# Kernel optimization log

Hardware: AMD Instinct MI355X
Metric: run time of the kernel (lower is better)

The kernel has to match this reference:

```python
import jax, jax.numpy as jnp
import numpy as np

C_CURV = 1.0          # Poincare ball curvature
EPS = 1e-5
MAX_NORM = (1.0 - 1e-4) / np.sqrt(C_CURV)


def _artanh(x):
    x = jnp.clip(x, -1.0 + 1e-5, 1.0 - 1e-5)
    return 0.5 * (jnp.log1p(x) - jnp.log1p(-x))


def _expmap0(v):
    # v: [N,C,H,W]; norm over channel dim per spatial location
    n = jnp.maximum(jnp.linalg.norm(v, axis=1, keepdims=True), EPS)
    sc = np.sqrt(C_CURV)
    return jnp.tanh(sc * n) * v / (sc * n)


def _logmap0(y):
    n = jnp.maximum(jnp.linalg.norm(y, axis=1, keepdims=True), EPS)
    sc = np.sqrt(C_CURV)
    return _artanh(sc * n) * y / (sc * n)


def _project(y):
    # clamp back inside the ball
    n = jnp.maximum(jnp.linalg.norm(y, axis=1, keepdims=True), EPS)
    return jnp.where(n > MAX_NORM, y * (MAX_NORM / n), y)


def _conv3x3(u, w, b):
    y = jax.lax.conv_general_dilated(u, w, window_strides=(1, 1),
                                     padding=((1, 1), (1, 1)),
                                     dimension_numbers=('NCHW', 'OIHW', 'NCHW'))
    return y + b[None, :, None, None]


def _hconv(x, w, b):
    # HConvolution2d: tangent-space conv around origin
    return _project(_expmap0(_conv3x3(_logmap0(x), w, b)))


def _hbn(x, gamma, beta):
    # HBatchNorm2d: Euclidean BN in the tangent space at the origin (training stats)
    u = _logmap0(x)
    m = u.mean(axis=(0, 2, 3), keepdims=True)
    v = u.var(axis=(0, 2, 3), keepdims=True)
    u = (u - m) / jnp.sqrt(v + 1e-5)
    u = u * gamma[None, :, None, None] + beta[None, :, None, None]
    return _project(_expmap0(u))


def _hrelu(x):
    return _project(_expmap0(jax.nn.relu(_logmap0(x))))


def setup_inputs() -> dict:
    key = jax.random.key(0)
    ks = jax.random.split(key, 8)
    N, Cin, Cmid, Cout, H, W = 8, 32, 32, 32, 256, 256
    # input point on the Poincare ball
    x = _project(_expmap0(0.1 * jax.random.normal(ks[0], (N, Cin, H, W), jnp.float32)))
    fan1 = Cin * 9
    fan2 = Cmid * 9
    w1 = jax.random.normal(ks[1], (Cmid, Cin, 3, 3), jnp.float32) / np.sqrt(fan1)
    b1 = jnp.zeros((Cmid,), jnp.float32)
    g1 = jnp.ones((Cmid,), jnp.float32)
    beta1 = jnp.zeros((Cmid,), jnp.float32)
    w2 = jax.random.normal(ks[2], (Cout, Cmid, 3, 3), jnp.float32) / np.sqrt(fan2)
    b2 = jnp.zeros((Cout,), jnp.float32)
    g2 = jnp.ones((Cout,), jnp.float32)
    beta2 = jnp.zeros((Cout,), jnp.float32)
    return {"x": x, "w1": w1, "b1": b1, "g1": g1, "beta1": beta1,
            "w2": w2, "b2": b2, "g2": g2, "beta2": beta2}


def reference(x, w1, b1, g1, beta1, w2, b2, g2, beta2):
    out = _hconv(x, w1, b1)
    out = _hbn(out, g1, beta1)
    out = _hrelu(out)
    out = _hconv(out, w2, b2)
    out = _hbn(out, g2, beta2)
    out = _hrelu(out)
    return out
```

## Files before the change

### kernel.cpp

```cpp
#include <hip/hip_runtime.h>
#include <math.h>

#define HWDIM 256
#define CH 32
#define NB 8
#define TILE 16
#define NLOC (NB*HWDIM*HWDIM)
#define R_CLAMP 4.9517189f
#define MAXN 0.9999f
#define BN_EPS 1e-5f
#define EPSF 1e-5f
#define TPB 2
#define GRIDC 1024
#define OST 264

typedef __attribute__((ext_vector_type(8))) _Float16 half8;
typedef __attribute__((ext_vector_type(4))) _Float16 half4;
typedef __attribute__((ext_vector_type(4))) float floatx4;

__device__ __forceinline__ float artanh_fast(float n) {
    float t = fminf(n, 1.0f - 1e-5f);
    return 0.5f * __logf(__fdividef(1.0f + t, 1.0f - t));
}

__global__ __launch_bounds__(256) void wprep_kernel(
    const float* __restrict__ w1, const float* __restrict__ w2,
    _Float16* __restrict__ wp1, _Float16* __restrict__ wp2)
{
    int idx = blockIdx.x * 256 + threadIdx.x;
    if (idx >= 2*CH*CH*9) return;
    int s = idx >= CH*CH*9;
    int id = idx - s*(CH*CH*9);
    const float* w = s ? w2 : w1;
    _Float16* wp = s ? wp2 : wp1;
    int j  = id & 7;
    int r  = id >> 3;
    int co = r & 31;
    int og = r >> 5;
    int g  = og & 3;
    int o  = og >> 2;
    int ci = g*8 + j;
    wp[id] = (_Float16)w[(co*CH + ci)*9 + o];
}

template<int STAGE>
__device__ __forceinline__ void stage_loc(const void* __restrict__ srcv, int bz,
                                          int gh, int gw, bool inb,
                                          _Float16* base, const float* __restrict__ scsh)
{
    if (!inb) {
        half8 z = {0,0,0,0,0,0,0,0};
        #pragma unroll
        for (int g = 0; g < 4; g++) *(half8*)(base + g*144) = z;
        return;
    }
    float v[CH]; float n2 = 0.f;
    if (STAGE == 1) {
        const float* p = (const float*)srcv + ((size_t)bz*CH << 16) + gh*HWDIM + gw;
        #pragma unroll
        for (int c = 0; c < CH; c++) { float t0 = p[(size_t)c << 16]; v[c] = t0; n2 = fmaf(t0, t0, n2); }
        float n = fmaxf(sqrtf(n2), EPSF);
        float f = __fdividef(artanh_fast(n), n);
        #pragma unroll
        for (int g = 0; g < 4; g++) {
            half8 hv;
            #pragma unroll
            for (int j = 0; j < 8; j++) hv[j] = (_Float16)(v[g*8 + j] * f);
            *(half8*)(base + g*144) = hv;
        }
    } else {
        const _Float16* p = (const _Float16*)srcv + (((size_t)bz << 16) + gh*HWDIM + gw)*CH;
        half8 raw[4];
        #pragma unroll
        for (int k = 0; k < 4; k++) raw[k] = *(const half8*)(p + 8*k);
        #pragma unroll
        for (int c = 0; c < CH; c++) {
            float t0 = fmaf((float)raw[c>>3][c&7], scsh[c], scsh[CH + c]);
            v[c] = t0; n2 = fmaf(t0, t0, n2);
        }
        float n = sqrtf(n2);
        float f = (n > R_CLAMP) ? __fdividef(R_CLAMP, n) : 1.0f;
        #pragma unroll
        for (int g = 0; g < 4; g++) {
            half8 hv;
            #pragma unroll
            for (int j = 0; j < 8; j++) hv[j] = (_Float16)fmaxf(v[g*8 + j]*f, 0.0f);
            *(half8*)(base + g*144) = hv;
        }
    }
}

template<int STAGE>
__global__ __launch_bounds__(256) void conv_mfma_kernel(
    const void* __restrict__ srcv,
    const _Float16* __restrict__ wp,
    const float* __restrict__ bias,
    const float* __restrict__ scsh,
    _Float16* __restrict__ dst,
    float* __restrict__ partials)
{
    __shared__ _Float16 ah[10368];
    __shared__ float red[4][64];

    const int tid = threadIdx.x;
    const int b   = blockIdx.x;
    const int bz  = b & 7;
    const int tb  = b >> 3;
    const int by  = tb >> 3;
    const int bx0 = (tb & 7) * TPB;
    const int h0  = by*TILE - 1;
    const int wbase = bx0*TILE - 1;

    const int sy0 = tid / 18, sx0 = tid - sy0*18;
    const int gh0 = h0 + sy0;
    const bool row0 = (gh0 >= 0) & (gh0 < HWDIM);
    const bool has1 = tid < 68;
    const int l1 = tid + 256;
    const int sy1 = l1 / 18, sx1 = l1 - sy1*18;
    const int gh1 = h0 + sy1;
    const bool row1 = has1 & (gh1 >= 0) & (gh1 < HWDIM);
    _Float16* const base0 = ah + ((sy0*4)*18 + sx0)*8;
    _Float16* const base1 = ah + ((sy1*4)*18 + sx1)*8;

    const int lane = tid & 63, wave = tid >> 6;
    const int xx = lane & 15, q = lane >> 4;

    float bs[8];
    #pragma unroll
    for (int r = 0; r < 4; r++) { bs[r] = bias[q*4+r]; bs[4+r] = bias[q*4+r+16]; }
    float sv[8], qv[8];
    #pragma unroll
    for (int k = 0; k < 8; k++) { sv[k] = 0.f; qv[k] = 0.f; }

    #pragma unroll 1
    for (int j = 0; j < TPB; j++) {
        {
            int gw0 = wbase + j*TILE + sx0;
            bool in0 = row0 & (gw0 >= 0) & (gw0 < HWDIM);
            stage_loc<STAGE>(srcv, bz, gh0, gw0, in0, base0, scsh);
        }
        if (has1) {
            int gw1 = wbase + j*TILE + sx1;
            bool in1 = row1 & (gw1 >= 0) & (gw1 < HWDIM);
            stage_loc<STAGE>(srcv, bz, gh1, gw1, in1, base1, scsh);
        }
        __syncthreads();

        floatx4 acc[4][2];
        #pragma unroll
        for (int i = 0; i < 4; i++) {
            acc[i][0] = (floatx4){0.f,0.f,0.f,0.f};
            acc[i][1] = (floatx4){0.f,0.f,0.f,0.f};
        }
        __builtin_amdgcn_s_setprio(1);
        #pragma unroll
        for (int dx = 0; dx < 3; dx++) {
            half8 af[6];
            #pragma unroll
            for (int yy = 0; yy < 6; yy++)
                af[yy] = *(const half8*)(ah + (((wave*4+yy)*4 + q)*18 + xx + dx)*8);
            #pragma unroll
            for (int dy = 0; dy < 3; dy++) {
                const int o = dy*3 + dx;
                const _Float16* wb = wp + (size_t)((o*4 + q)*32)*8;
                half8 wf0 = *(const half8*)(wb + xx*8);
                half8 wf1 = *(const half8*)(wb + (xx+16)*8);
                #pragma unroll
                for (int i = 0; i < 4; i++) {
                    acc[i][0] = __builtin_amdgcn_mfma_f32_16x16x32_f16(wf0, af[i+dy], acc[i][0], 0,0,0);
                    acc[i][1] = __builtin_amdgcn_mfma_f32_16x16x32_f16(wf1, af[i+dy], acc[i][1], 0,0,0);
                }
            }
        }
        __builtin_amdgcn_s_setprio(0);

        _Float16* dp = dst + (((size_t)bz << 16) + (size_t)(by*TILE)*HWDIM + (bx0 + j)*TILE + xx)*CH + q*4;
        #pragma unroll
        for (int i = 0; i < 4; i++) {
            float n2 = 0.f;
            #pragma unroll
            for (int r = 0; r < 4; r++) {
                acc[i][0][r] += bs[r];
                acc[i][1][r] += bs[4+r];
                n2 = fmaf(acc[i][0][r], acc[i][0][r], n2);
                n2 = fmaf(acc[i][1][r], acc[i][1][r], n2);
            }
            n2 += __shfl_xor(n2, 16, 64);
            n2 += __shfl_xor(n2, 32, 64);
            float nn = sqrtf(n2);
            float f = (nn > R_CLAMP) ? __fdividef(R_CLAMP, nn) : 1.0f;
            half4 o0, o1;
            #pragma unroll
            for (int r = 0; r < 4; r++) {
                float a0 = acc[i][0][r] * f;
                float a1 = acc[i][1][r] * f;
                sv[r]   += a0; qv[r]   = fmaf(a0, a0, qv[r]);
                sv[4+r] += a1; qv[4+r] = fmaf(a1, a1, qv[4+r]);
                o0[r] = (_Float16)a0; o1[r] = (_Float16)a1;
            }
            _Float16* a = dp + (size_t)(wave*4 + i)*HWDIM*CH;
            *(half4*)(a)      = o0;
            *(half4*)(a + 16) = o1;
        }
        __syncthreads();
    }

    #pragma unroll
    for (int k = 0; k < 8; k++) {
        #pragma unroll
        for (int m = 1; m < 16; m <<= 1) {
            sv[k] += __shfl_xor(sv[k], m, 64);
            qv[k] += __shfl_xor(qv[k], m, 64);
        }
    }
    if (xx == 0) {
        #pragma unroll
        for (int r = 0; r < 4; r++) {
            red[wave][q*4+r]        = sv[r];
            red[wave][16 + q*4+r]   = sv[4+r];
            red[wave][32 + q*4+r]   = qv[r];
            red[wave][48 + q*4+r]   = qv[4+r];
        }
    }
    __syncthreads();
    if (tid < 64) {
        float s = red[0][tid] + red[1][tid] + red[2][tid] + red[3][tid];
        partials[(size_t)tid*GRIDC + b] = s;
    }
}

__global__ __launch_bounds__(256) void finalize_kernel(
    const float* __restrict__ partials,
    const float* __restrict__ g, const float* __restrict__ beta,
    float* __restrict__ scsh)
{
    __shared__ float ss[256], sq[256];
    const int c = blockIdx.x;
    const int tid = threadIdx.x;
    float s = 0.f, q = 0.f;
    for (int b = tid; b < GRIDC; b += 256) {
        s += partials[(size_t)c*GRIDC + b];
        q += partials[(size_t)(CH + c)*GRIDC + b];
    }
    ss[tid] = s; sq[tid] = q;
    __syncthreads();
    for (int st = 128; st > 0; st >>= 1) {
        if (tid < st) { ss[tid] += ss[tid+st]; sq[tid] += sq[tid+st]; }
        __syncthreads();
    }
    if (tid == 0) {
        const float NS = (float)NLOC;
        float mean = ss[0] / NS;
        float var = fmaxf(sq[0] / NS - mean*mean, 0.0f);
        float sc = g[c] / sqrtf(var + BN_EPS);
        scsh[c] = sc;
        scsh[CH + c] = beta[c] - mean*sc;
    }
}

__global__ __launch_bounds__(256) void out_kernel(
    const _Float16* __restrict__ t4c, const float* __restrict__ scsh,
    float* __restrict__ out)
{
    __shared__ float outb[16*OST];
    const int w = threadIdx.x;
    const int h = blockIdx.x, n = blockIdx.y;
    const _Float16* p = t4c + (((size_t)n << 16) + (size_t)h*HWDIM + w)*CH;
    half8 raw[4];
    #pragma unroll
    for (int k = 0; k < 4; k++) raw[k] = *(const half8*)(p + 8*k);
    float u[CH]; float n2 = 0.f;
    #pragma unroll
    for (int c = 0; c < CH; c++) {
        float t = fmaf((float)raw[c>>3][c&7], scsh[c], scsh[CH+c]);
        u[c] = t; n2 = fmaf(t, t, n2);
    }
    float nn = sqrtf(n2);
    float f = (nn > R_CLAMP) ? __fdividef(R_CLAMP, nn) : 1.0f;
    float r2 = 0.f;
    #pragma unroll
    for (int c = 0; c < CH; c++) { float r = fmaxf(u[c]*f, 0.0f); u[c] = r; r2 = fmaf(r, r, r2); }
    float rn = fmaxf(sqrtf(r2), EPSF);
    float a = __expf(2.0f * rn);
    float th = __fdividef(a - 1.0f, a + 1.0f);
    float s = __fdividef(fminf(th, MAXN), rn);
    #pragma unroll
    for (int c = 0; c < CH; c++) u[c] *= s;

    #pragma unroll
    for (int hf = 0; hf < 2; hf++) {
        if (hf) __syncthreads();
        #pragma unroll
        for (int c = 0; c < 16; c++) outb[c*OST + w] = u[hf*16 + c];
        __syncthreads();
        int co = threadIdx.x >> 4, seg = threadIdx.x & 15;
        const float* row = outb + co*OST + seg*16;
        float* gp = out + ((size_t)(n*CH + hf*16 + co) << 16) + (size_t)h*HWDIM + seg*16;
        #pragma unroll
        for (int k = 0; k < 4; k++) *(floatx4*)(gp + 4*k) = *(const floatx4*)(row + 4*k);
    }
}

extern "C" void kernel_launch(void* const* d_in, const int* in_sizes, int n_in,
                              void* d_out, int out_size, void* d_ws, size_t ws_size,
                              hipStream_t stream)
{
    const float* x   = (const float*)d_in[0];
    const float* w1  = (const float*)d_in[1];
    const float* b1  = (const float*)d_in[2];
    const float* g1  = (const float*)d_in[3];
    const float* be1 = (const float*)d_in[4];
    const float* w2  = (const float*)d_in[5];
    const float* b2  = (const float*)d_in[6];
    const float* g2  = (const float*)d_in[7];
    const float* be2 = (const float*)d_in[8];
    float* outf = (float*)d_out;

    char* ws = (char*)d_ws;
    _Float16* wp1   = (_Float16*)ws;
    _Float16* wp2   = wp1 + 9216;
    float* partials = (float*)(ws + 36864);
    float* scsh1    = (float*)(ws + 36864 + 262144);
    float* scsh2    = scsh1 + 64;
    _Float16* t1c   = (_Float16*)(scsh2 + 64);
    _Float16* t4c   = t1c + (size_t)NLOC*CH;

    wprep_kernel<<<72, 256, 0, stream>>>(w1, w2, wp1, wp2);

    conv_mfma_kernel<1><<<GRIDC, 256, 0, stream>>>(x, wp1, b1, scsh1, t1c, partials);
    finalize_kernel<<<32, 256, 0, stream>>>(partials, g1, be1, scsh1);
    conv_mfma_kernel<2><<<GRIDC, 256, 0, stream>>>(t1c, wp2, b2, scsh1, t4c, partials);
    finalize_kernel<<<32, 256, 0, stream>>>(partials, g2, be2, scsh2);
    out_kernel<<<dim3(HWDIM, NB), 256, 0, stream>>>(t4c, scsh2, outf);
}
```

Measured before the change: 202.9 us.

## Fuse BN finalize into conv kernels via atomics and last-block reduction

Removes the two separate finalize kernels. Each conv block now atomically adds its per-channel sums into a small global buffer, and the last block to finish (found with an atomic counter) computes the BN scale and shift. The counters and accumulators are zeroed in the weight-prep kernel. The staging loop is also rewritten as a generic strided loop instead of the two fixed slots. This saves two launches and the partials round-trip, at the cost of float atomic contention and non-deterministic summation order.

```diff
diff --git a/kernel.cpp b/kernel.cpp
--- a/kernel.cpp
+++ b/kernel.cpp
@@ -25,9 +25,17 @@
 
 __global__ __launch_bounds__(256) void wprep_kernel(
     const float* __restrict__ w1, const float* __restrict__ w2,
-    _Float16* __restrict__ wp1, _Float16* __restrict__ wp2)
+    _Float16* __restrict__ wp1, _Float16* __restrict__ wp2,
+    float* __restrict__ gstatA, unsigned* __restrict__ ctrA,
+    float* __restrict__ gstatB, unsigned* __restrict__ ctrB)
 {
     int idx = blockIdx.x * 256 + threadIdx.x;
+    if (blockIdx.x == 0) {
+        int tid = threadIdx.x;
+        if (tid < 64) { gstatA[tid] = 0.f; gstatB[tid] = 0.f; }
+        if (tid == 64) *ctrA = 0u;
+        if (tid == 65) *ctrB = 0u;
+    }
     if (idx >= 2*CH*CH*9) return;
     int s = idx >= CH*CH*9;
     int id = idx - s*(CH*CH*9);
@@ -44,63 +52,20 @@
 }
 
 template<int STAGE>
-__device__ __forceinline__ void stage_loc(const void* __restrict__ srcv, int bz,
-                                          int gh, int gw, bool inb,
-                                          _Float16* base, const float* __restrict__ scsh)
-{
-    if (!inb) {
-        half8 z = {0,0,0,0,0,0,0,0};
-        #pragma unroll
-        for (int g = 0; g < 4; g++) *(half8*)(base + g*144) = z;
-        return;
-    }
-    float v[CH]; float n2 = 0.f;
-    if (STAGE == 1) {
-        const float* p = (const float*)srcv + ((size_t)bz*CH << 16) + gh*HWDIM + gw;
-        #pragma unroll
-        for (int c = 0; c < CH; c++) { float t0 = p[(size_t)c << 16]; v[c] = t0; n2 = fmaf(t0, t0, n2); }
-        float n = fmaxf(sqrtf(n2), EPSF);
-        float f = __fdividef(artanh_fast(n), n);
-        #pragma unroll
-        for (int g = 0; g < 4; g++) {
-            half8 hv;
-            #pragma unroll
-            for (int j = 0; j < 8; j++) hv[j] = (_Float16)(v[g*8 + j] * f);
-            *(half8*)(base + g*144) = hv;
-        }
-    } else {
-        const _Float16* p = (const _Float16*)srcv + (((size_t)bz << 16) + gh*HWDIM + gw)*CH;
-        half8 raw[4];
-        #pragma unroll
-        for (int k = 0; k < 4; k++) raw[k] = *(const half8*)(p + 8*k);
-        #pragma unroll
-        for (int c = 0; c < CH; c++) {
-            float t0 = fmaf((float)raw[c>>3][c&7], scsh[c], scsh[CH + c]);
-            v[c] = t0; n2 = fmaf(t0, t0, n2);
-        }
-        float n = sqrtf(n2);
-        float f = (n > R_CLAMP) ? __fdividef(R_CLAMP, n) : 1.0f;
-        #pragma unroll
-        for (int g = 0; g < 4; g++) {
-            half8 hv;
-            #pragma unroll
-            for (int j = 0; j < 8; j++) hv[j] = (_Float16)fmaxf(v[g*8 + j]*f, 0.0f);
-            *(half8*)(base + g*144) = hv;
-        }
-    }
-}
-
-template<int STAGE>
 __global__ __launch_bounds__(256) void conv_mfma_kernel(
     const void* __restrict__ srcv,
     const _Float16* __restrict__ wp,
     const float* __restrict__ bias,
-    const float* __restrict__ scsh,
+    const float* __restrict__ scsh_in,
     _Float16* __restrict__ dst,
-    float* __restrict__ partials)
+    float* __restrict__ gstat,
+    unsigned* __restrict__ ctr,
+    const float* __restrict__ gamma, const float* __restrict__ beta,
+    float* __restrict__ scsh_out)
 {
     __shared__ _Float16 ah[10368];
     __shared__ float red[4][64];
+    __shared__ bool lastf;
 
     const int tid = threadIdx.x;
     const int b   = blockIdx.x;
@@ -111,17 +76,6 @@
     const int h0  = by*TILE - 1;
     const int wbase = bx0*TILE - 1;
 
-    const int sy0 = tid / 18, sx0 = tid - sy0*18;
-    const int gh0 = h0 + sy0;
-    const bool row0 = (gh0 >= 0) & (gh0 < HWDIM);
-    const bool has1 = tid < 68;
-    const int l1 = tid + 256;
-    const int sy1 = l1 / 18, sx1 = l1 - sy1*18;
-    const int gh1 = h0 + sy1;
-    const bool row1 = has1 & (gh1 >= 0) & (gh1 < HWDIM);
-    _Float16* const base0 = ah + ((sy0*4)*18 + sx0)*8;
-    _Float16* const base1 = ah + ((sy1*4)*18 + sx1)*8;
-
     const int lane = tid & 63, wave = tid >> 6;
     const int xx = lane & 15, q = lane >> 4;
 
@@ -134,15 +88,52 @@
 
     #pragma unroll 1
     for (int j = 0; j < TPB; j++) {
-        {
-            int gw0 = wbase + j*TILE + sx0;
-            bool in0 = row0 & (gw0 >= 0) & (gw0 < HWDIM);
-            stage_loc<STAGE>(srcv, bz, gh0, gw0, in0, base0, scsh);
-        }
-        if (has1) {
-            int gw1 = wbase + j*TILE + sx1;
-            bool in1 = row1 & (gw1 >= 0) & (gw1 < HWDIM);
-            stage_loc<STAGE>(srcv, bz, gh1, gw1, in1, base1, scsh);
+        const int w0 = wbase + j*TILE;
+        #pragma unroll 1
+        for (int loc = tid; loc < 324; loc += 256) {
+            int y = loc / 18, x = loc - y*18;
+            int gh = h0 + y, gw = w0 + x;
+            _Float16* base = ah + ((y*4)*18 + x)*8;
+            if (gh < 0 || gh >= HWDIM || gw < 0 || gw >= HWDIM) {
+                half8 z = {0,0,0,0,0,0,0,0};
+                #pragma unroll
+                for (int g = 0; g < 4; g++) *(half8*)(base + g*144) = z;
+                continue;
+            }
+            float v[CH]; float n2 = 0.f;
+            if (STAGE == 1) {
+                const float* p = (const float*)srcv + ((size_t)bz*CH << 16) + gh*HWDIM + gw;
+                #pragma unroll
+                for (int c = 0; c < CH; c++) { float t0 = p[(size_t)c << 16]; v[c] = t0; n2 = fmaf(t0, t0, n2); }
+                float n = fmaxf(sqrtf(n2), EPSF);
+                float f = __fdividef(artanh_fast(n), n);
+                #pragma unroll
+                for (int g = 0; g < 4; g++) {
+                    half8 hv;
+                    #pragma unroll
+                    for (int jj = 0; jj < 8; jj++) hv[jj] = (_Float16)(v[g*8 + jj] * f);
+                    *(half8*)(base + g*144) = hv;
+                }
+            } else {
+                const _Float16* p = (const _Float16*)srcv + (((size_t)bz << 16) + gh*HWDIM + gw)*CH;
+                half8 raw[4];
+                #pragma unroll
+                for (int k = 0; k < 4; k++) raw[k] = *(const half8*)(p + 8*k);
+                #pragma unroll
+                for (int c = 0; c < CH; c++) {
+                    float t0 = fmaf((float)raw[c>>3][c&7], scsh_in[c], scsh_in[CH + c]);
+                    v[c] = t0; n2 = fmaf(t0, t0, n2);
+                }
+                float n = sqrtf(n2);
+                float f = (n > R_CLAMP) ? __fdividef(R_CLAMP, n) : 1.0f;
+                #pragma unroll
+                for (int g = 0; g < 4; g++) {
+                    half8 hv;
+                    #pragma unroll
+                    for (int jj = 0; jj < 8; jj++) hv[jj] = (_Float16)fmaxf(v[g*8 + jj]*f, 0.0f);
+                    *(half8*)(base + g*144) = hv;
+                }
+            }
         }
         __syncthreads();
 
@@ -225,36 +216,24 @@
     __syncthreads();
     if (tid < 64) {
         float s = red[0][tid] + red[1][tid] + red[2][tid] + red[3][tid];
-        partials[(size_t)tid*GRIDC + b] = s;
-    }
-}
-
-__global__ __launch_bounds__(256) void finalize_kernel(
-    const float* __restrict__ partials,
-    const float* __restrict__ g, const float* __restrict__ beta,
-    float* __restrict__ scsh)
-{
-    __shared__ float ss[256], sq[256];
-    const int c = blockIdx.x;
-    const int tid = threadIdx.x;
-    float s = 0.f, q = 0.f;
-    for (int b = tid; b < GRIDC; b += 256) {
-        s += partials[(size_t)c*GRIDC + b];
-        q += partials[(size_t)(CH + c)*GRIDC + b];
-    }
-    ss[tid] = s; sq[tid] = q;
+        __hip_atomic_fetch_add(&gstat[tid], s, __ATOMIC_RELAXED, __HIP_MEMORY_SCOPE_AGENT);
+    }
     __syncthreads();
-    for (int st = 128; st > 0; st >>= 1) {
-        if (tid < st) { ss[tid] += ss[tid+st]; sq[tid] += sq[tid+st]; }
-        __syncthreads();
-    }
     if (tid == 0) {
+        __threadfence();
+        unsigned t = __hip_atomic_fetch_add(ctr, 1u, __ATOMIC_ACQ_REL, __HIP_MEMORY_SCOPE_AGENT);
+        lastf = (t == (unsigned)(GRIDC - 1));
+    }
+    __syncthreads();
+    if (lastf && tid < 32) {
+        float sum = __hip_atomic_load(&gstat[tid],      __ATOMIC_RELAXED, __HIP_MEMORY_SCOPE_AGENT);
+        float sq  = __hip_atomic_load(&gstat[32 + tid], __ATOMIC_RELAXED, __HIP_MEMORY_SCOPE_AGENT);
         const float NS = (float)NLOC;
-        float mean = ss[0] / NS;
-        float var = fmaxf(sq[0] / NS - mean*mean, 0.0f);
-        float sc = g[c] / sqrtf(var + BN_EPS);
-        scsh[c] = sc;
-        scsh[CH + c] = beta[c] - mean*sc;
+        float mean = sum / NS;
+        float var = fmaxf(sq / NS - mean*mean, 0.0f);
+        float sc = gamma[tid] / sqrtf(var + BN_EPS);
+        scsh_out[tid] = sc;
+        scsh_out[CH + tid] = beta[tid] - mean*sc;
     }
 }
 
@@ -319,17 +298,18 @@
     char* ws = (char*)d_ws;
     _Float16* wp1   = (_Float16*)ws;
     _Float16* wp2   = wp1 + 9216;
-    float* partials = (float*)(ws + 36864);
-    float* scsh1    = (float*)(ws + 36864 + 262144);
-    float* scsh2    = scsh1 + 64;
-    _Float16* t1c   = (_Float16*)(scsh2 + 64);
+    float* gstatA   = (float*)(ws + 36864);
+    unsigned* ctrA  = (unsigned*)(ws + 37120);
+    float* gstatB   = (float*)(ws + 37184);
+    unsigned* ctrB  = (unsigned*)(ws + 37440);
+    float* scsh1    = (float*)(ws + 37504);
+    float* scsh2    = (float*)(ws + 37760);
+    _Float16* t1c   = (_Float16*)(ws + 38016);
     _Float16* t4c   = t1c + (size_t)NLOC*CH;
 
-    wprep_kernel<<<72, 256, 0, stream>>>(w1, w2, wp1, wp2);
-
-    conv_mfma_kernel<1><<<GRIDC, 256, 0, stream>>>(x, wp1, b1, scsh1, t1c, partials);
-    finalize_kernel<<<32, 256, 0, stream>>>(partials, g1, be1, scsh1);
-    conv_mfma_kernel<2><<<GRIDC, 256, 0, stream>>>(t1c, wp2, b2, scsh1, t4c, partials);
-    finalize_kernel<<<32, 256, 0, stream>>>(partials, g2, be2, scsh2);
+    wprep_kernel<<<72, 256, 0, stream>>>(w1, w2, wp1, wp2, gstatA, ctrA, gstatB, ctrB);
+
+    conv_mfma_kernel<1><<<GRIDC, 256, 0, stream>>>(x,   wp1, b1, scsh1, t1c, gstatA, ctrA, g1, be1, scsh1);
+    conv_mfma_kernel<2><<<GRIDC, 256, 0, stream>>>(t1c, wp2, b2, scsh1, t4c, gstatB, ctrB, g2, be2, scsh2);
     out_kernel<<<dim3(HWDIM, NB), 256, 0, stream>>>(t4c, scsh2, outf);
 }
```

Result: slower. 372.4 us (+83.5%).
